# Kernel optimization log

Measured on AMD Instinct MI355X. Metric: run time of the kernel, lower is better.

Reference implementation:

```python
import jax, jax.numpy as jnp
import numpy as np

B, V = 256, 128000


def setup_inputs() -> dict:
    key = jax.random.key(0)
    k1, k2, k3, k4, k5 = jax.random.split(key, 5)
    logits = jax.random.normal(k1, (B, V), dtype=jnp.float32) * 2.0
    temperatures = jax.random.uniform(k2, (B,), dtype=jnp.float32, minval=0.5, maxval=1.5)
    top_ps = jax.random.uniform(k3, (B,), dtype=jnp.float32, minval=0.7, maxval=1.0)
    top_ks = jax.random.randint(k4, (B,), 1, 101, dtype=jnp.int32)
    min_ps = jax.random.uniform(k5, (B,), dtype=jnp.float32, minval=0.0, maxval=0.1)
    return {"logits": logits, "temperatures": temperatures, "top_ps": top_ps,
            "top_ks": top_ks, "min_ps": min_ps}


def reference(logits, temperatures, top_ps, top_ks, min_ps):
    # temperature scaling + softmax (forward path with is_all_greedy=False)
    logits = logits.astype(jnp.float32) / temperatures[:, None]
    probs = jax.nn.softmax(logits, axis=-1)  # [B, V]

    # descending sort of probabilities, keep permutation for un-sorting
    order = jnp.argsort(-probs, axis=-1)                      # [B, V]
    probs_sort = jnp.take_along_axis(probs, order, axis=-1)   # [B, V]
    csum = jnp.cumsum(probs_sort, axis=-1)                    # cumsum BEFORE masking (matches torch)

    ranks = jnp.arange(V, dtype=jnp.int32)[None, :]
    probs_sort = jnp.where(ranks >= top_ks[:, None], 0.0, probs_sort)          # top-k mask
    probs_sort = jnp.where(csum - probs_sort > top_ps[:, None], 0.0, probs_sort)  # top-p mask
    # need_min_p_sampling=False in forward, so min_ps is unused (kept for signature parity)

    # multinomial(num_samples=1) over unnormalized masked probs == categorical on log-weights
    logw = jnp.where(probs_sort > 0, jnp.log(probs_sort), -jnp.inf)
    sampled = jax.random.categorical(jax.random.key(42), logw, axis=-1)  # [B]
    next_ids = jnp.take_along_axis(order, sampled[:, None], axis=-1).reshape(-1)
    return next_ids
```

## Files before the change

### kernel.cpp

```cpp
#include <hip/hip_runtime.h>
#include <stdint.h>
#include <math.h>

#define BB 256
#define VV 128000
#define NV4 (VV / 4)
#define NBINS 8192
#define CAP 512
#define KMAX 100
#define TPB 1024
#define NWAVE (TPB / 64)

__device__ __forceinline__ uint32_t threefry_xor_bits(uint32_t x0, uint32_t x1) {
    const uint32_t k0 = 0u, k1 = 42u;
    const uint32_t k2 = k0 ^ k1 ^ 0x1BD11BDAu;
    uint32_t ks[3] = {k0, k1, k2};
    const int rotA[4] = {13, 15, 26, 6};
    const int rotB[4] = {17, 29, 16, 24};
    x0 += ks[0];
    x1 += ks[1];
#pragma unroll
    for (int g = 0; g < 5; g++) {
        const int* rot = (g & 1) ? rotB : rotA;
#pragma unroll
        for (int i = 0; i < 4; i++) {
            x0 += x1;
            x1 = (x1 << rot[i]) | (x1 >> (32 - rot[i]));
            x1 ^= x0;
        }
        x0 += ks[(g + 1) % 3];
        x1 += ks[(g + 2) % 3] + (uint32_t)(g + 1);
    }
    return x0 ^ x1;
}

__device__ __forceinline__ uint32_t flip_key(uint32_t ub) {
    return (ub & 0x80000000u) ? ~ub : (ub | 0x80000000u);
}

__global__ __launch_bounds__(TPB) void sampler_kernel(
    const float* __restrict__ logits,
    const float* __restrict__ temps,
    const float* __restrict__ top_ps,
    const int* __restrict__ top_ks,
    int* __restrict__ out) {
    __shared__ uint32_t hist[NBINS];
    __shared__ uint32_t scan_u[TPB];
    __shared__ float wv[NWAVE];
    __shared__ float cand_l[CAP];
    __shared__ int cand_idx[CAP];
    __shared__ float cand_p[CAP];
    __shared__ float sort_p[KMAX];
    __shared__ int sort_idx[KMAX];
    __shared__ float csum_s[KMAX];
    __shared__ float red_val[128];
    __shared__ int red_idx[128];
    __shared__ int s_cnt;
    __shared__ uint32_t s_tkey;
    __shared__ float s_m, s_lmax, s_z;

    const int b = blockIdx.x;
    const int tid = threadIdx.x;
    const int lane = tid & 63;
    const int wave = tid >> 6;
    const float T = temps[b];
    const float4* row4 = (const float4*)(logits + (size_t)b * VV);

    for (int i = tid; i < NBINS; i += TPB) hist[i] = 0;
    if (tid == 0) s_cnt = 0;
    __syncthreads();

    float lmax = -INFINITY;
    for (int i = tid; i < NV4; i += TPB) {
        float4 v = row4[i];
        float a0 = v.x, a1 = v.y, a2 = v.z, a3 = v.w;
        lmax = fmaxf(lmax, fmaxf(fmaxf(a0, a1), fmaxf(a2, a3)));
        atomicAdd(&hist[flip_key(__float_as_uint(a0)) >> 19], 1u);
        atomicAdd(&hist[flip_key(__float_as_uint(a1)) >> 19], 1u);
        atomicAdd(&hist[flip_key(__float_as_uint(a2)) >> 19], 1u);
        atomicAdd(&hist[flip_key(__float_as_uint(a3)) >> 19], 1u);
    }
    for (int s = 32; s > 0; s >>= 1) lmax = fmaxf(lmax, __shfl_down(lmax, s));
    if (lane == 0) wv[wave] = lmax;
    __syncthreads();
    if (tid == 0) {
        float M = wv[0];
        for (int w = 1; w < NWAVE; w++) M = fmaxf(M, wv[w]);
        s_lmax = M;
        s_m = M / T;
    }
    __syncthreads();

    uint32_t csum_chunk = 0;
#pragma unroll
    for (int j = 0; j < 8; j++) csum_chunk += hist[tid * 8 + j];
    scan_u[tid] = csum_chunk;
    __syncthreads();
    for (int s = 1; s < TPB; s <<= 1) {
        uint32_t v = scan_u[tid];
        uint32_t w = (tid + s < TPB) ? scan_u[tid + s] : 0u;
        __syncthreads();
        scan_u[tid] = v + w;
        __syncthreads();
    }
    {
        uint32_t St = scan_u[tid];
        uint32_t St1 = (tid + 1 < TPB) ? scan_u[tid + 1] : 0u;
        if (St >= (uint32_t)KMAX && St1 < (uint32_t)KMAX) {
            uint32_t running = St1;
            for (int jj = tid * 8 + 7; jj >= tid * 8; jj--) {
                running += hist[jj];
                if (running >= (uint32_t)KMAX) {
                    s_tkey = (uint32_t)jj << 19;
                    break;
                }
            }
        }
    }
    __syncthreads();

    const float m = s_m;
    const float lmax_g = s_lmax;
    const uint32_t tkey = s_tkey;
    const float c1 = 1.4426950408889634f / T;

    float zpart = 0.f;
    for (int i = tid; i < NV4; i += TPB) {
        float4 v = row4[i];
        float a[4] = {v.x, v.y, v.z, v.w};
#pragma unroll
        for (int j = 0; j < 4; j++) {
            float l = a[j];
            zpart += exp2f((l - lmax_g) * c1);
            if (flip_key(__float_as_uint(l)) >= tkey) {
                int slot = atomicAdd(&s_cnt, 1);
                if (slot < CAP) {
                    cand_l[slot] = l;
                    cand_idx[slot] = i * 4 + j;
                }
            }
        }
    }
    for (int s = 32; s > 0; s >>= 1) zpart += __shfl_down(zpart, s);
    __syncthreads();
    if (lane == 0) wv[wave] = zpart;
    __syncthreads();
    if (tid == 0) {
        float Zs = wv[0];
        for (int w = 1; w < NWAVE; w++) Zs += wv[w];
        s_z = Zs;
    }
    __syncthreads();
    const float Z = s_z;
    const int C = (s_cnt < CAP) ? s_cnt : CAP;
    __syncthreads();

    float my_pn = 0.f;
    int my_idx = 0;
    if (tid < C) {
        float x = cand_l[tid] / T;
        float p = expf(x - m);
        my_pn = p / Z;
        my_idx = cand_idx[tid];
        cand_p[tid] = my_pn;
    }
    __syncthreads();
    if (tid < C) {
        int r = 0;
        for (int c = 0; c < C; c++) {
            float pc = cand_p[c];
            int ic = cand_idx[c];
            if (pc > my_pn || (pc == my_pn && ic < my_idx)) r++;
        }
        if (r < KMAX) {
            sort_p[r] = my_pn;
            sort_idx[r] = my_idx;
        }
    }
    __syncthreads();

    if (tid == 0) {
        float c = 0.f;
        for (int r = 0; r < KMAX; r++) {
            c += sort_p[r];
            csum_s[r] = c;
        }
    }
    __syncthreads();

    const int topk = top_ks[b];
    const float topp = top_ps[b];
    float val = -INFINITY;
    if (tid < KMAX && tid < topk) {
        float p = sort_p[tid];
        if (!(csum_s[tid] - p > topp)) {
            float lw = logf(p);
            uint32_t i = (uint32_t)b * (uint32_t)VV + (uint32_t)tid;
            uint32_t bits = threefry_xor_bits(0u, i);
            uint32_t fb = (bits >> 9) | 0x3F800000u;
            float f = __uint_as_float(fb) - 1.0f;
            const float TINY = 1.17549435082228751e-38f;
            float u = fmaxf(TINY, __fadd_rn(__fmul_rn(f, 1.0f - TINY), TINY));
            float g = -logf(-logf(u));
            val = g + lw;
        }
    }
    if (tid < 128) {
        red_val[tid] = (tid < KMAX) ? val : -INFINITY;
        red_idx[tid] = tid;
    }
    __syncthreads();
    for (int s = 64; s > 0; s >>= 1) {
        if (tid < s) {
            float v1 = red_val[tid], v2 = red_val[tid + s];
            int i1 = red_idx[tid], i2 = red_idx[tid + s];
            if (v2 > v1 || (v2 == v1 && i2 < i1)) {
                red_val[tid] = v2;
                red_idx[tid] = i2;
            }
        }
        __syncthreads();
    }
    if (tid == 0) out[b] = sort_idx[red_idx[0]];
}

extern "C" void kernel_launch(void* const* d_in, const int* in_sizes, int n_in,
                              void* d_out, int out_size, void* d_ws, size_t ws_size,
                              hipStream_t stream) {
    const float* logits = (const float*)d_in[0];
    const float* temps = (const float*)d_in[1];
    const float* top_ps = (const float*)d_in[2];
    const int* top_ks = (const int*)d_in[3];
    int* out = (int*)d_out;
    sampler_kernel<<<BB, TPB, 0, stream>>>(logits, temps, top_ps, top_ks, out);
}
```

Before: 233.3 us.

## Replace histogram radix-select with fixed-threshold single-pass candidate collection

Measured after the change: 238.8 us. 2.3% more time.

```diff
diff --git a/kernel.cpp b/kernel.cpp
--- a/kernel.cpp
+++ b/kernel.cpp
@@ -5,11 +5,19 @@
 #define BB 256
 #define VV 128000
 #define NV4 (VV / 4)
-#define NBINS 8192
-#define CAP 512
+#define NHALF4 (NV4 / 2)
+#define CAPG 512
 #define KMAX 100
 #define TPB 1024
-#define NWAVE (TPB / 64)
+#define TPC 512
+#define THR 6.0f
+#define LOG2E 1.4426950408889634f
+
+#define WS_CNT_OFF 0
+#define WS_Z_OFF 1024
+#define WS_CL_OFF 3072
+#define WS_CI_OFF (3072 + BB * CAPG * 4)
+#define WS_NEED (size_t)(3072 + BB * CAPG * 8)
 
 __device__ __forceinline__ uint32_t threefry_xor_bits(uint32_t x0, uint32_t x1) {
     const uint32_t k0 = 0u, k1 = 42u;
@@ -34,151 +42,18 @@
     return x0 ^ x1;
 }
 
-__device__ __forceinline__ uint32_t flip_key(uint32_t ub) {
-    return (ub & 0x80000000u) ? ~ub : (ub | 0x80000000u);
-}
-
-__global__ __launch_bounds__(TPB) void sampler_kernel(
-    const float* __restrict__ logits,
-    const float* __restrict__ temps,
-    const float* __restrict__ top_ps,
-    const int* __restrict__ top_ks,
-    int* __restrict__ out) {
-    __shared__ uint32_t hist[NBINS];
-    __shared__ uint32_t scan_u[TPB];
-    __shared__ float wv[NWAVE];
-    __shared__ float cand_l[CAP];
-    __shared__ int cand_idx[CAP];
-    __shared__ float cand_p[CAP];
-    __shared__ float sort_p[KMAX];
-    __shared__ int sort_idx[KMAX];
-    __shared__ float csum_s[KMAX];
-    __shared__ float red_val[128];
-    __shared__ int red_idx[128];
-    __shared__ int s_cnt;
-    __shared__ uint32_t s_tkey;
-    __shared__ float s_m, s_lmax, s_z;
-
-    const int b = blockIdx.x;
-    const int tid = threadIdx.x;
-    const int lane = tid & 63;
-    const int wave = tid >> 6;
-    const float T = temps[b];
-    const float4* row4 = (const float4*)(logits + (size_t)b * VV);
-
-    for (int i = tid; i < NBINS; i += TPB) hist[i] = 0;
-    if (tid == 0) s_cnt = 0;
-    __syncthreads();
-
-    float lmax = -INFINITY;
-    for (int i = tid; i < NV4; i += TPB) {
-        float4 v = row4[i];
-        float a0 = v.x, a1 = v.y, a2 = v.z, a3 = v.w;
-        lmax = fmaxf(lmax, fmaxf(fmaxf(a0, a1), fmaxf(a2, a3)));
-        atomicAdd(&hist[flip_key(__float_as_uint(a0)) >> 19], 1u);
-        atomicAdd(&hist[flip_key(__float_as_uint(a1)) >> 19], 1u);
-        atomicAdd(&hist[flip_key(__float_as_uint(a2)) >> 19], 1u);
-        atomicAdd(&hist[flip_key(__float_as_uint(a3)) >> 19], 1u);
-    }
-    for (int s = 32; s > 0; s >>= 1) lmax = fmaxf(lmax, __shfl_down(lmax, s));
-    if (lane == 0) wv[wave] = lmax;
-    __syncthreads();
-    if (tid == 0) {
-        float M = wv[0];
-        for (int w = 1; w < NWAVE; w++) M = fmaxf(M, wv[w]);
-        s_lmax = M;
-        s_m = M / T;
-    }
-    __syncthreads();
-
-    uint32_t csum_chunk = 0;
-#pragma unroll
-    for (int j = 0; j < 8; j++) csum_chunk += hist[tid * 8 + j];
-    scan_u[tid] = csum_chunk;
-    __syncthreads();
-    for (int s = 1; s < TPB; s <<= 1) {
-        uint32_t v = scan_u[tid];
-        uint32_t w = (tid + s < TPB) ? scan_u[tid + s] : 0u;
-        __syncthreads();
-        scan_u[tid] = v + w;
-        __syncthreads();
-    }
-    {
-        uint32_t St = scan_u[tid];
-        uint32_t St1 = (tid + 1 < TPB) ? scan_u[tid + 1] : 0u;
-        if (St >= (uint32_t)KMAX && St1 < (uint32_t)KMAX) {
-            uint32_t running = St1;
-            for (int jj = tid * 8 + 7; jj >= tid * 8; jj--) {
-                running += hist[jj];
-                if (running >= (uint32_t)KMAX) {
-                    s_tkey = (uint32_t)jj << 19;
-                    break;
-                }
-            }
-        }
-    }
-    __syncthreads();
-
-    const float m = s_m;
-    const float lmax_g = s_lmax;
-    const uint32_t tkey = s_tkey;
-    const float c1 = 1.4426950408889634f / T;
-
-    float zpart = 0.f;
-    for (int i = tid; i < NV4; i += TPB) {
-        float4 v = row4[i];
-        float a[4] = {v.x, v.y, v.z, v.w};
-#pragma unroll
-        for (int j = 0; j < 4; j++) {
-            float l = a[j];
-            zpart += exp2f((l - lmax_g) * c1);
-            if (flip_key(__float_as_uint(l)) >= tkey) {
-                int slot = atomicAdd(&s_cnt, 1);
-                if (slot < CAP) {
-                    cand_l[slot] = l;
-                    cand_idx[slot] = i * 4 + j;
-                }
-            }
-        }
-    }
-    for (int s = 32; s > 0; s >>= 1) zpart += __shfl_down(zpart, s);
-    __syncthreads();
-    if (lane == 0) wv[wave] = zpart;
-    __syncthreads();
-    if (tid == 0) {
-        float Zs = wv[0];
-        for (int w = 1; w < NWAVE; w++) Zs += wv[w];
-        s_z = Zs;
-    }
-    __syncthreads();
-    const float Z = s_z;
-    const int C = (s_cnt < CAP) ? s_cnt : CAP;
-    __syncthreads();
-
-    float my_pn = 0.f;
-    int my_idx = 0;
-    if (tid < C) {
-        float x = cand_l[tid] / T;
-        float p = expf(x - m);
-        my_pn = p / Z;
-        my_idx = cand_idx[tid];
-        cand_p[tid] = my_pn;
-    }
-    __syncthreads();
-    if (tid < C) {
-        int r = 0;
-        for (int c = 0; c < C; c++) {
-            float pc = cand_p[c];
-            int ic = cand_idx[c];
-            if (pc > my_pn || (pc == my_pn && ic < my_idx)) r++;
-        }
-        if (r < KMAX) {
-            sort_p[r] = my_pn;
-            sort_idx[r] = my_idx;
-        }
-    }
-    __syncthreads();
-
+__device__ __forceinline__ float wave_maxf(float v) {
+    for (int s = 32; s > 0; s >>= 1) v = fmaxf(v, __shfl_down(v, s));
+    return v;
+}
+__device__ __forceinline__ float wave_sumf(float v) {
+    for (int s = 32; s > 0; s >>= 1) v += __shfl_down(v, s);
+    return v;
+}
+
+__device__ void common_tail(int b, int tid, const float* sort_p, const int* sort_idx,
+                            float* csum_s, float* red_val, int* red_idx,
+                            float topp, int topk, int* out) {
     if (tid == 0) {
         float c = 0.f;
         for (int r = 0; r < KMAX; r++) {
@@ -187,16 +62,13 @@
         }
     }
     __syncthreads();
-
-    const int topk = top_ks[b];
-    const float topp = top_ps[b];
     float val = -INFINITY;
     if (tid < KMAX && tid < topk) {
         float p = sort_p[tid];
         if (!(csum_s[tid] - p > topp)) {
             float lw = logf(p);
-            uint32_t i = (uint32_t)b * (uint32_t)VV + (uint32_t)tid;
-            uint32_t bits = threefry_xor_bits(0u, i);
+            uint32_t idx = (uint32_t)b * (uint32_t)VV + (uint32_t)tid;
+            uint32_t bits = threefry_xor_bits(0u, idx);
             uint32_t fb = (bits >> 9) | 0x3F800000u;
             float f = __uint_as_float(fb) - 1.0f;
             const float TINY = 1.17549435082228751e-38f;
@@ -222,6 +94,327 @@
         __syncthreads();
     }
     if (tid == 0) out[b] = sort_idx[red_idx[0]];
+}
+
+template <int NT>
+__device__ void fallback_fill(const float* row, float T, int tid,
+                              float* wv, int* iwv, float* sort_p, int* sort_idx,
+                              float* s_f , int* s_i ) {
+    const int lane = tid & 63, wave = tid >> 6;
+    const int NW = NT / 64;
+    float lm = -INFINITY;
+    for (int j = tid; j < VV; j += NT) lm = fmaxf(lm, row[j]);
+    lm = wave_maxf(lm);
+    if (lane == 0) wv[wave] = lm;
+    __syncthreads();
+    if (tid == 0) {
+        float M = wv[0];
+        for (int w = 1; w < NW; w++) M = fmaxf(M, wv[w]);
+        s_f[0] = M;
+    }
+    __syncthreads();
+    const float m = s_f[0] / T;
+    float zp = 0.f;
+    for (int j = tid; j < VV; j += NT) zp += expf(row[j] / T - m);
+    zp = wave_sumf(zp);
+    __syncthreads();
+    if (lane == 0) wv[wave] = zp;
+    __syncthreads();
+    if (tid == 0) {
+        float Zs = wv[0];
+        for (int w = 1; w < NW; w++) Zs += wv[w];
+        s_f[1] = Zs;
+    }
+    __syncthreads();
+    const float Z = s_f[1];
+    float prevP = INFINITY;
+    int prevJ = -1;
+    for (int r = 0; r < KMAX; r++) {
+        float bp = -1.f;
+        int bj = 0x7FFFFFFF;
+        for (int j = tid; j < VV; j += NT) {
+            float p = expf(row[j] / T - m);
+            bool elig = (p < prevP) || (p == prevP && j > prevJ);
+            if (elig && (p > bp || (p == bp && j < bj))) {
+                bp = p;
+                bj = j;
+            }
+        }
+        for (int s = 32; s > 0; s >>= 1) {
+            float op = __shfl_down(bp, s);
+            int oj = __shfl_down(bj, s);
+            if (op > bp || (op == bp && oj < bj)) {
+                bp = op;
+                bj = oj;
+            }
+        }
+        if (lane == 0) {
+            wv[wave] = bp;
+            iwv[wave] = bj;
+        }
+        __syncthreads();
+        if (tid == 0) {
+            float P = wv[0];
+            int J = iwv[0];
+            for (int w = 1; w < NW; w++)
+                if (wv[w] > P || (wv[w] == P && iwv[w] < J)) {
+                    P = wv[w];
+                    J = iwv[w];
+                }
+            sort_p[r] = P / Z;
+            sort_idx[r] = J;
+            s_f[1] = P;
+            s_i[0] = J;
+        }
+        __syncthreads();
+        prevP = s_f[1];
+        prevJ = s_i[0];
+        __syncthreads();
+    }
+}
+
+__global__ void init_kernel(int* wcnt) {
+    if (threadIdx.x < BB) wcnt[threadIdx.x] = 0;
+}
+
+__global__ __launch_bounds__(TPB, 8) void pass_kernel(
+    const float* __restrict__ logits, const float* __restrict__ temps,
+    int* __restrict__ wcnt, float* __restrict__ wz,
+    float* __restrict__ wcl, int* __restrict__ wci) {
+    __shared__ float wv[TPB / 64];
+    const int blk = blockIdx.x;
+    const int b = blk >> 1, half = blk & 1;
+    const int tid = threadIdx.x, lane = tid & 63, wave = tid >> 6;
+    const float T = temps[b];
+    const float c1 = LOG2E / T;
+    const float4* row4 = (const float4*)(logits + (size_t)b * VV) + half * NHALF4;
+    const int base4 = half * NHALF4;
+
+    float z = 0.f;
+    int i = tid;
+    for (; i + 3 * TPB < NHALF4; i += 4 * TPB) {
+        float4 v0 = row4[i];
+        float4 v1 = row4[i + TPB];
+        float4 v2 = row4[i + 2 * TPB];
+        float4 v3 = row4[i + 3 * TPB];
+        float a[16] = {v0.x, v0.y, v0.z, v0.w, v1.x, v1.y, v1.z, v1.w,
+                       v2.x, v2.y, v2.z, v2.w, v3.x, v3.y, v3.z, v3.w};
+#pragma unroll
+        for (int j = 0; j < 16; j++) {
+            float l = a[j];
+            z += exp2f(l * c1);
+            if (l >= THR) {
+                int slot = atomicAdd(&wcnt[b], 1);
+                if (slot < CAPG) {
+                    wcl[b * CAPG + slot] = l;
+                    wci[b * CAPG + slot] = (base4 + i + (j >> 2) * TPB) * 4 + (j & 3);
+                }
+            }
+        }
+    }
+    for (; i < NHALF4; i += TPB) {
+        float4 v = row4[i];
+        float a[4] = {v.x, v.y, v.z, v.w};
+#pragma unroll
+        for (int j = 0; j < 4; j++) {
+            float l = a[j];
+            z += exp2f(l * c1);
+            if (l >= THR) {
+                int slot = atomicAdd(&wcnt[b], 1);
+                if (slot < CAPG) {
+                    wcl[b * CAPG + slot] = l;
+                    wci[b * CAPG + slot] = (base4 + i) * 4 + j;
+                }
+            }
+        }
+    }
+    z = wave_sumf(z);
+    if (lane == 0) wv[wave] = z;
+    __syncthreads();
+    if (tid == 0) {
+        float Z = wv[0];
+        for (int w = 1; w < TPB / 64; w++) Z += wv[w];
+        wz[2 * b + half] = Z;
+    }
+}
+
+__global__ __launch_bounds__(TPC) void tail_kernel(
+    const float* __restrict__ logits, const float* __restrict__ temps,
+    const float* __restrict__ top_ps, const int* __restrict__ top_ks,
+    const int* __restrict__ wcnt, const float* __restrict__ wz,
+    const float* __restrict__ wcl, const int* __restrict__ wci,
+    int* __restrict__ out) {
+    __shared__ float cand_p[CAPG];
+    __shared__ int cand_i[CAPG];
+    __shared__ float sort_p[KMAX];
+    __shared__ int sort_idx[KMAX];
+    __shared__ float csum_s[KMAX];
+    __shared__ float red_val[128];
+    __shared__ int red_idx[128];
+    __shared__ float wv[TPC / 64];
+    __shared__ int iwv[TPC / 64];
+    __shared__ float s_f[2];
+    __shared__ int s_i[1];
+
+    const int b = blockIdx.x, tid = threadIdx.x, lane = tid & 63, wave = tid >> 6;
+    const float T = temps[b];
+    const float c1 = LOG2E / T;
+    const int cnt = wcnt[b];
+    const float* row = logits + (size_t)b * VV;
+
+    if (cnt >= KMAX && cnt <= CAPG) {
+        const int C = cnt;
+        float myl = -INFINITY;
+        int myi = 0;
+        if (tid < C) {
+            myl = wcl[b * CAPG + tid];
+            myi = wci[b * CAPG + tid];
+        }
+        float v = wave_maxf(myl);
+        if (lane == 0) wv[wave] = v;
+        __syncthreads();
+        if (tid == 0) {
+            float M = wv[0];
+            for (int w = 1; w < TPC / 64; w++) M = fmaxf(M, wv[w]);
+            s_f[0] = M;
+        }
+        __syncthreads();
+        const float lmax = s_f[0];
+        const float m = lmax / T;
+        const float Z = (wz[2 * b] + wz[2 * b + 1]) * exp2f(-lmax * c1);
+        float my_pn = 0.f;
+        if (tid < C) {
+            float x = myl / T;
+            float p = expf(x - m);
+            my_pn = p / Z;
+            cand_p[tid] = my_pn;
+            cand_i[tid] = myi;
+        }
+        __syncthreads();
+        if (tid < C) {
+            int r = 0;
+            for (int c = 0; c < C; c++) {
+                float pc = cand_p[c];
+                int ic = cand_i[c];
+                if (pc > my_pn || (pc == my_pn && ic < myi)) r++;
+            }
+            if (r < KMAX) {
+                sort_p[r] = my_pn;
+                sort_idx[r] = myi;
+            }
+        }
+        __syncthreads();
+    } else {
+        fallback_fill<TPC>(row, T, tid, wv, iwv, sort_p, sort_idx, s_f, s_i);
+    }
+
+    common_tail(b, tid, sort_p, sort_idx, csum_s, red_val, red_idx,
+                top_ps[b], top_ks[b], out);
+}
+
+__global__ __launch_bounds__(TPB) void fused_kernel(
+    const float* __restrict__ logits, const float* __restrict__ temps,
+    const float* __restrict__ top_ps, const int* __restrict__ top_ks,
+    int* __restrict__ out) {
+    __shared__ float cl[CAPG];
+    __shared__ int ci[CAPG];
+    __shared__ float cand_p[CAPG];
+    __shared__ int cand_i[CAPG];
+    __shared__ float sort_p[KMAX];
+    __shared__ int sort_idx[KMAX];
+    __shared__ float csum_s[KMAX];
+    __shared__ float red_val[128];
+    __shared__ int red_idx[128];
+    __shared__ float wv[TPB / 64];
+    __shared__ int iwv[TPB / 64];
+    __shared__ float s_f[2];
+    __shared__ int s_i[1];
+    __shared__ int s_cnt;
+
+    const int b = blockIdx.x, tid = threadIdx.x, lane = tid & 63, wave = tid >> 6;
+    const float T = temps[b];
+    const float c1 = LOG2E / T;
+    const float* row = logits + (size_t)b * VV;
+    const float4* row4 = (const float4*)row;
+
+    if (tid == 0) s_cnt = 0;
+    __syncthreads();
+    float z = 0.f, lmax = -INFINITY;
+    for (int i = tid; i < NV4; i += TPB) {
+        float4 v = row4[i];
+        float a[4] = {v.x, v.y, v.z, v.w};
+#pragma unroll
+        for (int j = 0; j < 4; j++) {
+            float l = a[j];
+            lmax = fmaxf(lmax, l);
+            z += exp2f(l * c1);
+            if (l >= THR) {
+                int slot = atomicAdd(&s_cnt, 1);
+                if (slot < CAPG) {
+                    cl[slot] = l;
+                    ci[slot] = i * 4 + j;
+                }
+            }
+        }
+    }
+    lmax = wave_maxf(lmax);
+    if (lane == 0) wv[wave] = lmax;
+    __syncthreads();
+    if (tid == 0) {
+        float M = wv[0];
+        for (int w = 1; w < TPB / 64; w++) M = fmaxf(M, wv[w]);
+        s_f[0] = M;
+    }
+    __syncthreads();
+    const float lm = s_f[0];
+    z = wave_sumf(z);
+    __syncthreads();
+    if (lane == 0) wv[wave] = z;
+    __syncthreads();
+    if (tid == 0) {
+        float Zs = wv[0];
+        for (int w = 1; w < TPB / 64; w++) Zs += wv[w];
+        s_f[1] = Zs;
+    }
+    __syncthreads();
+    const float Zraw = s_f[1];
+    const int cnt = s_cnt;
+    __syncthreads();
+
+    if (cnt >= KMAX && cnt <= CAPG) {
+        const int C = cnt;
+        const float m = lm / T;
+        const float Z = Zraw * exp2f(-lm * c1);
+        float my_pn = 0.f;
+        int myi = 0;
+        if (tid < C) {
+            float x = cl[tid] / T;
+            float p = expf(x - m);
+            my_pn = p / Z;
+            myi = ci[tid];
+            cand_p[tid] = my_pn;
+            cand_i[tid] = myi;
+        }
+        __syncthreads();
+        if (tid < C) {
+            int r = 0;
+            for (int c = 0; c < C; c++) {
+                float pc = cand_p[c];
+                int icx = cand_i[c];
+                if (pc > my_pn || (pc == my_pn && icx < myi)) r++;
+            }
+            if (r < KMAX) {
+                sort_p[r] = my_pn;
+                sort_idx[r] = myi;
+            }
+        }
+        __syncthreads();
+    } else {
+        fallback_fill<TPB>(row, T, tid, wv, iwv, sort_p, sort_idx, s_f, s_i);
+    }
+
+    common_tail(b, tid, sort_p, sort_idx, csum_s, red_val, red_idx,
+                top_ps[b], top_ks[b], out);
 }
 
 extern "C" void kernel_launch(void* const* d_in, const int* in_sizes, int n_in,
@@ -232,5 +425,18 @@
     const float* top_ps = (const float*)d_in[2];
     const int* top_ks = (const int*)d_in[3];
     int* out = (int*)d_out;
-    sampler_kernel<<<BB, TPB, 0, stream>>>(logits, temps, top_ps, top_ks, out);
-}
+
+    if (ws_size >= WS_NEED) {
+        char* wsb = (char*)d_ws;
+        int* wcnt = (int*)(wsb + WS_CNT_OFF);
+        float* wz = (float*)(wsb + WS_Z_OFF);
+        float* wcl = (float*)(wsb + WS_CL_OFF);
+        int* wci = (int*)(wsb + WS_CI_OFF);
+        init_kernel<<<1, 256, 0, stream>>>(wcnt);
+        pass_kernel<<<BB * 2, TPB, 0, stream>>>(logits, temps, wcnt, wz, wcl, wci);
+        tail_kernel<<<BB, TPC, 0, stream>>>(logits, temps, top_ps, top_ks,
+                                            wcnt, wz, wcl, wci, out);
+    } else {
+        fused_kernel<<<BB, TPB, 0, stream>>>(logits, temps, top_ps, top_ks, out);
+    }
+}
```
